# Kernel tuning notes

Hardware: AMD Instinct MI355X
Metric: run time of the kernel (lower is better)

## Reference

```python
import jax, jax.numpy as jnp
import numpy as np
from jax import lax

# ---- custom-numeric primitives matching the torch Function classes ----

def _sign1(x):
    # torch.sign with sign(0) -> 1
    return jnp.where(x >= 0, jnp.ones_like(x), -jnp.ones_like(x))

bin_act = _sign1            # BinaryActivation.forward
bin_weight = _sign1         # WeightsToBinary.forward
round_bias = jnp.round      # BiasToInt.forward

C_IN, C_OUT, K = 14, 128, 7
H_MID = 2 * K               # h = k * 2 = 14
PAD = K // 2                # 3


def _conv(x, w, b, stride, pad, groups):
    y = lax.conv_general_dilated(
        x, w,
        window_strides=(stride, stride),
        padding=((pad, pad), (pad, pad)),
        dimension_numbers=("NCHW", "OIHW", "NCHW"),
        feature_group_count=groups,
    )
    return y + b[None, :, None, None]


def setup_inputs() -> dict:
    key = jax.random.key(0)
    ks = jax.random.split(key, 7)
    B, H, W = 8, 384, 384
    x = jax.random.normal(ks[0], (B, C_IN, H, W), dtype=jnp.float32)
    # latent float weights in roughly (-1, 1) like a trained BNN
    w1 = 0.5 * jax.random.normal(ks[1], (H_MID, 1, K, K), dtype=jnp.float32)      # depthwise, groups=C_IN
    b1 = 0.5 * jax.random.normal(ks[2], (H_MID,), dtype=jnp.float32)
    w2 = 0.5 * jax.random.normal(ks[3], (C_OUT, H_MID, 1, 1), dtype=jnp.float32)
    b2 = 0.5 * jax.random.normal(ks[4], (C_OUT,), dtype=jnp.float32)
    w3 = 0.5 * jax.random.normal(ks[5], (C_OUT, C_OUT, 1, 1), dtype=jnp.float32)
    b3 = 0.5 * jax.random.normal(ks[6], (C_OUT,), dtype=jnp.float32)
    return {"x": x, "w1": w1, "b1": b1, "w2": w2, "b2": b2, "w3": w3, "b3": b3}


def reference(x, w1, b1, w2, b2, w3, b3):
    # first=True: center then binarize input
    x = bin_act(x - jnp.mean(x))
    # conv1: depthwise k x k, stride 1, padding k//2 (same spatial)
    y = bin_act(_conv(x, bin_weight(w1), round_bias(b1), 1, PAD, C_IN))
    # conv2: 1x1 conv but padding k//2 (grows spatial by 2*PAD) -- quirk of source
    y = bin_act(_conv(y, bin_weight(w2), round_bias(b2), 1, PAD, 1))
    # conv3: 1x1 conv, stride 3, padding 1
    y = bin_act(_conv(y, bin_weight(w3), round_bias(b3), 3, 1, 1))
    return y
```

## Files before the change

kernel.cpp:

```cpp
#include <hip/hip_runtime.h>
#include <hip/hip_bf16.h>

#define NB     8
#define CIN    14
#define COUT   128
#define HW     384
#define OUT_HW 131
#define P      (OUT_HW*OUT_HW)
#define ROWS   390
#define NTOT   (NB*CIN*HW*HW)
#define NROWS  (NB*CIN*ROWS)
#define NPACK  1024
#define CAND_B 0.002f
#define NSLOT  8

typedef unsigned long long u64;
typedef unsigned int u32;

struct PackedW {
    uint4 padz;
    uint4 ringz;
    u64   w1pack[CIN];
    int   b1i[CIN];
};

__global__ __launch_bounds__(256) void pass1(
    const float* __restrict__ x, u64* __restrict__ xbin,
    double* __restrict__ part, u64* __restrict__ cands, u32* __restrict__ ccnt,
    const float* __restrict__ w1, const float* __restrict__ b1,
    const float* __restrict__ w2, const float* __restrict__ b2,
    const float* __restrict__ w3, const float* __restrict__ b3,
    uint4* __restrict__ zlut, PackedW* __restrict__ pw)
{
    const int tid  = threadIdx.x;
    const int lane = tid & 63;
    const int wv   = tid >> 6;

    if (blockIdx.x < NPACK) {
        const u64 lmlt = (1ull << lane) - 1ull;
        double s0 = 0.0, s1 = 0.0;
        const int wid = blockIdx.x * 4 + wv;
        for (int row = wid; row < NROWS; row += NPACK * 4) {
            int nc = row / ROWS;
            int rr = row - nc * ROWS;
            int r  = rr - 3;
            u64 v = 0;
            u32 running = 0;
            u64* crow = cands + (size_t)row * NSLOT;
            if (r >= 0 && r < HW) {
                const float* xr = x + ((size_t)nc * HW + r) * HW;
                float f0 = __builtin_nontemporal_load(xr + lane);
                float f1 = __builtin_nontemporal_load(xr + 64 + lane);
                float f2 = __builtin_nontemporal_load(xr + 128 + lane);
                float f3 = __builtin_nontemporal_load(xr + 192 + lane);
                float f4 = __builtin_nontemporal_load(xr + 256 + lane);
                float f5 = __builtin_nontemporal_load(xr + 320 + lane);
                s0 += ((double)f0 + (double)f1) + (double)f2;
                s1 += ((double)f3 + (double)f4) + (double)f5;
                u64 b0 = __ballot(f0 >= 0.f);
                u64 b1_ = __ballot(f1 >= 0.f);
                u64 b2_ = __ballot(f2 >= 0.f);
                u64 b3_ = __ballot(f3 >= 0.f);
                u64 b4_ = __ballot(f4 >= 0.f);
                u64 b5_ = __ballot(f5 >= 0.f);
                v = lane == 0 ? b0 : lane == 1 ? b1_ : lane == 2 ? b2_ :
                    lane == 3 ? b3_ : lane == 4 ? b4_ : lane == 5 ? b5_ : 0;

                const u32 pbase = (u32)row * 512u + (u32)lane;
                float fq[6] = {f0, f1, f2, f3, f4, f5};
                #pragma unroll
                for (int q = 0; q < 6; q++) {
                    u64 cq = __ballot(__builtin_fabsf(fq[q]) < CAND_B);
                    if (cq) {
                        if (__builtin_fabsf(fq[q]) < CAND_B) {
                            u32 slot = running + (u32)__popcll(cq & lmlt);
                            if (slot < NSLOT)
                                crow[slot] = ((u64)__float_as_uint(fq[q]) << 32)
                                           | (pbase + (u32)q * 64u);
                        }
                        running += (u32)__popcll(cq);
                    }
                }
            }
            if (lane < 8) xbin[(size_t)row * 8 + lane] = (lane < 6) ? v : 0;
            if (lane == 0) ccnt[row] = (running > NSLOT) ? NSLOT : running;
        }
        double s = s0 + s1;
        for (int off = 32; off; off >>= 1) s += __shfl_down(s, off);
        __shared__ double wsum[4];
        if (lane == 0) wsum[wv] = s;
        __syncthreads();
        if (tid == 0) part[blockIdx.x] = ((wsum[0] + wsum[1]) + (wsum[2] + wsum[3]));
        return;
    }

    if (blockIdx.x < NPACK + 64) {
        __shared__ u32  sw2e[COUT];
        __shared__ uint4 sw3p[COUT];
        __shared__ int  st3[COUT];
        if (tid < COUT) {
            u32 wb = 0;
            const float* w2r = w2 + tid * CIN;
            for (int c = 0; c < CIN; c++) wb |= (u32)(w2r[c] >= 0.f) << c;
            int b2i = (int)rintf(b2[tid]);
            sw2e[tid] = wb | ((u32)((CIN + b2i) >> 1) << 16);
            st3[tid] = (COUT + (int)rintf(b3[tid])) >> 1;
        }
        {
            int co = tid >> 1, half = tid & 1;
            const float* wr = w3 + co * COUT + half * 64;
            u64 mm = 0;
            #pragma unroll 8
            for (int c = 0; c < 64; c++) mm |= (u64)(wr[c] >= 0.f) << c;
            if (half == 0) { sw3p[co].x = (u32)mm; sw3p[co].y = (u32)(mm >> 32); }
            else           { sw3p[co].z = (u32)mm; sw3p[co].w = (u32)(mm >> 32); }
        }
        __syncthreads();

        const u32 y1v = (blockIdx.x - NPACK) * 256 + tid;
        u64 y2lo = 0, y2hi = 0;
        #pragma unroll 8
        for (int co = 0; co < 64; co++) {
            u32 e = sw2e[co];
            int p = __popc((y1v ^ e) & 0x3FFFu);
            y2lo |= (u64)(p <= ((int)e >> 16)) << co;
        }
        #pragma unroll 8
        for (int co = 0; co < 64; co++) {
            u32 e = sw2e[64 + co];
            int p = __popc((y1v ^ e) & 0x3FFFu);
            y2hi |= (u64)(p <= ((int)e >> 16)) << co;
        }
        u32 z[4] = {0, 0, 0, 0};
        #pragma unroll 4
        for (int co = 0; co < COUT; co++) {
            uint4 w = sw3p[co];
            int pp = (int)(__popcll(y2lo ^ (((u64)w.y << 32) | w.x))
                         + __popcll(y2hi ^ (((u64)w.w << 32) | w.z)));
            z[co >> 5] |= (u32)(pp <= st3[co]) << (co & 31);
        }
        zlut[y1v] = make_uint4(z[0], z[1], z[2], z[3]);
        return;
    }

    {
        __shared__ u64 sBorder[2], sPad[2], sRing[2];
        __shared__ u64 sw3lo[COUT], sw3hi[COUT];
        __shared__ int sb3[COUT];
        if (tid < COUT) {
            const float* wr = w3 + tid * COUT;
            u64 lo = 0, hi = 0;
            #pragma unroll 8
            for (int c = 0; c < 64; c++) lo |= (u64)(wr[c] >= 0.f) << c;
            #pragma unroll 8
            for (int c = 0; c < 64; c++) hi |= (u64)(wr[64 + c] >= 0.f) << c;
            sw3lo[tid] = lo; sw3hi[tid] = hi;
            int b2i = (int)rintf(b2[tid]);
            int b3i = (int)rintf(b3[tid]);
            sb3[tid] = b3i;
            u64 bb2 = __ballot(b2i >= 0);
            u64 bb3 = __ballot(b3i >= 0);
            if (lane == 0) { sBorder[wv] = bb2; sPad[wv] = bb3; }
        } else {
            int q = tid - COUT;
            if (q < CIN) {
                const float* wr = w1 + q * 49;
                u64 pk = 0;
                for (int c = 0; c < 49; c++) pk |= (u64)(wr[c] >= 0.f) << c;
                pw->w1pack[q] = pk;
                pw->b1i[q] = (int)rintf(b1[q]);
            }
        }
        __syncthreads();
        if (tid < COUT) {
            int s3 = COUT + sb3[tid]
                   - 2 * (int)(__popcll(sBorder[0] ^ sw3lo[tid]) + __popcll(sBorder[1] ^ sw3hi[tid]));
            u64 rb = __ballot(s3 >= 0);
            if (lane == 0) sRing[wv] = rb;
        }
        __syncthreads();
        if (tid == 0) {
            pw->padz  = make_uint4((u32)sPad[0],  (u32)(sPad[0] >> 32),  (u32)sPad[1],  (u32)(sPad[1] >> 32));
            pw->ringz = make_uint4((u32)sRing[0], (u32)(sRing[0] >> 32), (u32)sRing[1], (u32)(sRing[1] >> 32));
        }
    }
}

__global__ __launch_bounds__(256) void bnn_row(
    const u64* __restrict__ xbin, const PackedW* __restrict__ pw,
    const uint4* __restrict__ zlut, const double* __restrict__ part,
    const u64* __restrict__ cands, const u32* __restrict__ ccnt,
    float* __restrict__ out)
{
    __shared__ u64 xrows[CIN][7][8];
    __shared__ u32 zl[4][132];
    __shared__ u64 sw1[CIN];
    __shared__ int sb1[CIN];
    __shared__ double wsum[4];

    const int tid  = threadIdx.x;
    const int lane = tid & 63;
    const int wv   = tid >> 6;
    const u32 blk  = blockIdx.x;
    const u32 n = blk / OUT_HW;
    const u32 i = blk - n * OUT_HW;
    const bool interior = (i >= 2 && i <= 129);
    const int p0 = 3 * (int)i - 4;

    if (tid < CIN) { sw1[tid] = pw->w1pack[tid]; sb1[tid] = pw->b1i[tid]; }

    if (interior) {
        double t = 0.0;
        for (int q = tid; q < NPACK; q += 256) t += part[q];
        for (int off = 32; off; off >>= 1) t += __shfl_down(t, off);
        if (lane == 0) wsum[wv] = t;

        for (int t2 = tid; t2 < CIN * 56; t2 += 256) {
            int ci  = t2 / 56;
            int rem = t2 - ci * 56;
            int dy  = rem >> 3, w = rem & 7;
            xrows[ci][dy][w] =
                xbin[(((size_t)n * CIN + ci) * ROWS + (u32)(p0 + dy)) * 8 + w];
        }
    }
    __syncthreads();

    if (interior) {
        const float m = (float)((((wsum[0] + wsum[1]) + (wsum[2] + wsum[3]))
                                 / (double)NTOT));
        if (tid < CIN * 7) {
            int ci = tid / 7, dy = tid - ci * 7;
            u32 gr = ((u32)n * CIN + (u32)ci) * ROWS + (u32)(p0 + dy);
            u32 cnt = ccnt[gr];
            for (u32 s = 0; s < cnt; s++) {
                u64 e = cands[(size_t)gr * NSLOT + s];
                float v = __uint_as_float((u32)(e >> 32));
                bool bz = (v >= 0.f), bm = (v >= m);
                if (bz != bm) {
                    u32 pos = (u32)e;
                    xrows[ci][dy][(pos >> 6) & 7] ^= 1ull << (pos & 63);
                }
            }
        }
    }
    __syncthreads();

    if (tid < OUT_HW) {
        const int j = tid;
        uint4 zz;
        if (i == 0 || j == 0) {
            zz = pw->padz;
        } else if (!interior || j == 1 || j == 130) {
            zz = pw->ringz;
        } else {
            const int c0 = 3 * j - 7;
            const int lsh = (c0 < 0) ? 1 : 0;
            const int c0c = (c0 < 0) ? 0 : c0;
            const int k   = c0c >> 6;
            const int off = c0c & 63;
            const u64 selz = off ? ~0ull : 0ull;
            const int shl1 = (64 - off) & 63;
            u32 vm = 0x7Fu;
            if (c0 < 0)    vm = 0x7Eu;
            if (c0 == 380) vm = 0x0Fu;
            u64 vmrep = (u64)vm * 0x0000040810204081ull;
            u64 rmask = (1ull << 49) - 1;
            if (p0 < 3)   rmask &= ~((1ull << (7 * (3 - p0))) - 1);
            if (p0 > 380) rmask &= (1ull << (7 * (387 - p0))) - 1;
            const u64 M = vmrep & rmask;
            const int npop = (int)__popcll(M);

            u32 y1v = 0;
            #pragma unroll
            for (int ci = 0; ci < CIN; ci++) {
                u64 bits = 0;
                #pragma unroll
                for (int dy = 0; dy < 7; dy++) {
                    u64 w0 = xrows[ci][dy][k];
                    u64 w1 = xrows[ci][dy][k + 1];
                    u64 v = (w0 >> off) | ((w1 & selz) << shl1);
                    u32 b7 = ((u32)v << lsh) & 0x7Fu;
                    bits |= (u64)b7 << (7 * dy);
                }
                int T = sb1[ci] + npop - 2 * (int)__popcll((bits ^ sw1[ci]) & M);
                y1v |= (u32)(T >= 0) << ci;
            }
            zz = zlut[y1v];
        }
        zl[0][j] = zz.x; zl[1][j] = zz.y; zl[2][j] = zz.z; zl[3][j] = zz.w;
    }
    __syncthreads();

    const size_t base = (size_t)n * COUT * P + (size_t)i * OUT_HW;
    for (int co = wv; co < COUT; co += 4) {
        const u32 b = co & 31;
        const u32* zp = zl[co >> 5];
        float* op = out + base + (size_t)co * P;
        u32 wa = zp[lane], wb = zp[64 + lane];
        op[lane]      = ((wa >> b) & 1u) ? 1.0f : -1.0f;
        op[64 + lane] = ((wb >> b) & 1u) ? 1.0f : -1.0f;
        if (lane < 3) {
            u32 wc = zp[128 + lane];
            op[128 + lane] = ((wc >> b) & 1u) ? 1.0f : -1.0f;
        }
    }
}

extern "C" void kernel_launch(void* const* d_in, const int* in_sizes, int n_in,
                              void* d_out, int out_size, void* d_ws, size_t ws_size,
                              hipStream_t stream) {
    const float* x  = (const float*)d_in[0];
    const float* w1 = (const float*)d_in[1];
    const float* b1 = (const float*)d_in[2];
    const float* w2 = (const float*)d_in[3];
    const float* b2 = (const float*)d_in[4];
    const float* w3 = (const float*)d_in[5];
    const float* b3 = (const float*)d_in[6];
    float* out = (float*)d_out;

    double*  partials = (double*)d_ws;
    PackedW* pw       = (PackedW*)((char*)d_ws + 8448);
    uint4*   zlut     = (uint4*)((char*)d_ws + 16384);
    u64*     xbin     = (u64*)((char*)d_ws + 278528);
    u64*     cands    = (u64*)((char*)d_ws + 3074048);
    u32*     ccnt     = (u32*)((char*)d_ws + 5869568);

    pass1<<<NPACK + 64 + 1, 256, 0, stream>>>(x, xbin, partials, cands, ccnt,
                                              w1, b1, w2, b2, w3, b3, zlut, pw);
    bnn_row<<<NB * OUT_HW, 256, 0, stream>>>(xbin, pw, zlut, partials,
                                             cands, ccnt, out);
}
```

Measured before the change: 51.94 us.

## Split output unpack into separate kernel with coalesced vectorized float4 stores

```diff
diff --git a/kernel.cpp b/kernel.cpp
--- a/kernel.cpp
+++ b/kernel.cpp
@@ -7,15 +7,18 @@
 #define HW     384
 #define OUT_HW 131
 #define P      (OUT_HW*OUT_HW)
+#define TOTPIX (NB*P)
 #define ROWS   390
 #define NTOT   (NB*CIN*HW*HW)
 #define NROWS  (NB*CIN*ROWS)
 #define NPACK  1024
 #define CAND_B 0.002f
 #define NSLOT  8
+#define QELT   4291
 
 typedef unsigned long long u64;
 typedef unsigned int u32;
+typedef float f4 __attribute__((ext_vector_type(4)));
 
 struct PackedW {
     uint4 padz;
@@ -186,11 +189,11 @@
     }
 }
 
-__global__ __launch_bounds__(256) void bnn_row(
+__global__ __launch_bounds__(256) void conv_zrow(
     const u64* __restrict__ xbin, const PackedW* __restrict__ pw,
     const uint4* __restrict__ zlut, const double* __restrict__ part,
     const u64* __restrict__ cands, const u32* __restrict__ ccnt,
-    float* __restrict__ out)
+    u32* __restrict__ zws)
 {
     __shared__ u64 xrows[CIN][7][8];
     __shared__ u32 zl[4][132];
@@ -291,18 +294,53 @@
     }
     __syncthreads();
 
-    const size_t base = (size_t)n * COUT * P + (size_t)i * OUT_HW;
-    for (int co = wv; co < COUT; co += 4) {
-        const u32 b = co & 31;
-        const u32* zp = zl[co >> 5];
-        float* op = out + base + (size_t)co * P;
-        u32 wa = zp[lane], wb = zp[64 + lane];
-        op[lane]      = ((wa >> b) & 1u) ? 1.0f : -1.0f;
-        op[64 + lane] = ((wb >> b) & 1u) ? 1.0f : -1.0f;
-        if (lane < 3) {
-            u32 wc = zp[128 + lane];
-            op[128 + lane] = ((wc >> b) & 1u) ? 1.0f : -1.0f;
-        }
+    const u32 rbase = n * P + i * OUT_HW;
+    for (int t = tid; t < 4 * OUT_HW; t += 256) {
+        int qq = t / OUT_HW;
+        int j  = t - qq * OUT_HW;
+        zws[(size_t)qq * TOTPIX + rbase + j] = zl[qq][j];
+    }
+}
+
+__global__ __launch_bounds__(256) void unpack4(
+    const u32* __restrict__ zws, float* __restrict__ out)
+{
+    const u32 blk = blockIdx.x;
+    const u32 q   = blk >> 2;
+    const int s   = blk & 3;
+    const int tid = threadIdx.x;
+    const u32 n  = q >> 7, co = q & 127u, b = co & 31u;
+    const u32* zp = zws + (co >> 5) * TOTPIX + n * P;
+    float* op = out + (size_t)q * P;
+
+    const int lo = s * QELT;
+    const int hi = (lo + QELT < P) ? lo + QELT : P;
+    const int mis = (int)((q * (u32)P + (u32)lo) & 3u);
+    int a0 = mis ? (4 - mis) : 0;
+    if (lo + a0 > hi) a0 = hi - lo;
+
+    if (tid < a0) {
+        u32 w = zp[lo + tid];
+        op[lo + tid] = ((w >> b) & 1u) ? 1.0f : -1.0f;
+    }
+    const int start = lo + a0;
+    const int nch = (hi - start) >> 2;
+    for (int c = tid; c < nch; c += 256) {
+        int p0 = start + 4 * c;
+        u32 w0 = zp[p0], w1 = zp[p0 + 1], w2 = zp[p0 + 2], w3 = zp[p0 + 3];
+        f4 f;
+        f.x = ((w0 >> b) & 1u) ? 1.0f : -1.0f;
+        f.y = ((w1 >> b) & 1u) ? 1.0f : -1.0f;
+        f.z = ((w2 >> b) & 1u) ? 1.0f : -1.0f;
+        f.w = ((w3 >> b) & 1u) ? 1.0f : -1.0f;
+        *(f4*)(op + p0) = f;
+    }
+    const int done = start + 4 * nch;
+    const int rem  = hi - done;
+    if (tid >= 64 && tid < 64 + rem) {
+        int pix = done + (tid - 64);
+        u32 w = zp[pix];
+        op[pix] = ((w >> b) & 1u) ? 1.0f : -1.0f;
     }
 }
 
@@ -324,9 +362,11 @@
     u64*     xbin     = (u64*)((char*)d_ws + 278528);
     u64*     cands    = (u64*)((char*)d_ws + 3074048);
     u32*     ccnt     = (u32*)((char*)d_ws + 5869568);
+    u32*     zws      = (u32*)((char*)d_ws + 6045696);
 
     pass1<<<NPACK + 64 + 1, 256, 0, stream>>>(x, xbin, partials, cands, ccnt,
                                               w1, b1, w2, b2, w3, b3, zlut, pw);
-    bnn_row<<<NB * OUT_HW, 256, 0, stream>>>(xbin, pw, zlut, partials,
-                                             cands, ccnt, out);
+    conv_zrow<<<NB * OUT_HW, 256, 0, stream>>>(xbin, pw, zlut, partials,
+                                               cands, ccnt, zws);
+    unpack4<<<NB * COUT * 4, 256, 0, stream>>>(zws, out);
 }
```

Measured after the change: 54.52 us. 5.0% more time.

## Process two output rows per block to share input row loads

Applied to the files above, without the earlier changes.

```diff
diff --git a/kernel.cpp b/kernel.cpp
--- a/kernel.cpp
+++ b/kernel.cpp
@@ -13,6 +13,7 @@
 #define NPACK  1024
 #define CAND_B 0.002f
 #define NSLOT  8
+#define NPAIR  66
 
 typedef unsigned long long u64;
 typedef unsigned int u32;
@@ -192,8 +193,8 @@
     const u64* __restrict__ cands, const u32* __restrict__ ccnt,
     float* __restrict__ out)
 {
-    __shared__ u64 xrows[CIN][7][8];
-    __shared__ u32 zl[4][132];
+    __shared__ u64 xrows[CIN][10][8];
+    __shared__ u32 zl[4][2][132];
     __shared__ u64 sw1[CIN];
     __shared__ int sb1[CIN];
     __shared__ double wsum[4];
@@ -202,35 +203,37 @@
     const int lane = tid & 63;
     const int wv   = tid >> 6;
     const u32 blk  = blockIdx.x;
-    const u32 n = blk / OUT_HW;
-    const u32 i = blk - n * OUT_HW;
-    const bool interior = (i >= 2 && i <= 129);
-    const int p0 = 3 * (int)i - 4;
+    const u32 n  = blk / NPAIR;
+    const u32 ig = blk - n * NPAIR;
+    const int i0 = 2 * (int)ig;
+    const int nv = (i0 + 1 <= 130) ? 2 : 1;
+    const bool anyInt = (ig >= 1 && ig <= 64);
+    const int ps = 3 * i0 - 4;
 
     if (tid < CIN) { sw1[tid] = pw->w1pack[tid]; sb1[tid] = pw->b1i[tid]; }
 
-    if (interior) {
+    if (anyInt) {
         double t = 0.0;
         for (int q = tid; q < NPACK; q += 256) t += part[q];
         for (int off = 32; off; off >>= 1) t += __shfl_down(t, off);
         if (lane == 0) wsum[wv] = t;
 
-        for (int t2 = tid; t2 < CIN * 56; t2 += 256) {
-            int ci  = t2 / 56;
-            int rem = t2 - ci * 56;
+        for (int t2 = tid; t2 < CIN * 80; t2 += 256) {
+            int ci  = t2 / 80;
+            int rem = t2 - ci * 80;
             int dy  = rem >> 3, w = rem & 7;
             xrows[ci][dy][w] =
-                xbin[(((size_t)n * CIN + ci) * ROWS + (u32)(p0 + dy)) * 8 + w];
+                xbin[(((size_t)n * CIN + ci) * ROWS + (u32)(ps + dy)) * 8 + w];
         }
     }
     __syncthreads();
 
-    if (interior) {
+    if (anyInt) {
         const float m = (float)((((wsum[0] + wsum[1]) + (wsum[2] + wsum[3]))
                                  / (double)NTOT));
-        if (tid < CIN * 7) {
-            int ci = tid / 7, dy = tid - ci * 7;
-            u32 gr = ((u32)n * CIN + (u32)ci) * ROWS + (u32)(p0 + dy);
+        if (tid < CIN * 10) {
+            int ci = tid / 10, dy = tid - ci * 10;
+            u32 gr = ((u32)n * CIN + (u32)ci) * ROWS + (u32)(ps + dy);
             u32 cnt = ccnt[gr];
             for (u32 s = 0; s < cnt; s++) {
                 u64 e = cands[(size_t)gr * NSLOT + s];
@@ -245,14 +248,18 @@
     }
     __syncthreads();
 
-    if (tid < OUT_HW) {
-        const int j = tid;
+    for (int t = tid; t < nv * OUT_HW; t += 256) {
+        const int di = (t >= OUT_HW) ? 1 : 0;
+        const int j  = t - di * OUT_HW;
+        const int i  = i0 + di;
+        const bool interiorI = (i >= 2 && i <= 129);
         uint4 zz;
         if (i == 0 || j == 0) {
             zz = pw->padz;
-        } else if (!interior || j == 1 || j == 130) {
+        } else if (!interiorI || j == 1 || j == 130) {
             zz = pw->ringz;
         } else {
+            const int p0 = 3 * i - 4;
             const int c0 = 3 * j - 7;
             const int lsh = (c0 < 0) ? 1 : 0;
             const int c0c = (c0 < 0) ? 0 : c0;
@@ -269,6 +276,7 @@
             if (p0 > 380) rmask &= (1ull << (7 * (387 - p0))) - 1;
             const u64 M = vmrep & rmask;
             const int npop = (int)__popcll(M);
+            const int dyb = 3 * di;
 
             u32 y1v = 0;
             #pragma unroll
@@ -276,8 +284,8 @@
                 u64 bits = 0;
                 #pragma unroll
                 for (int dy = 0; dy < 7; dy++) {
-                    u64 w0 = xrows[ci][dy][k];
-                    u64 w1 = xrows[ci][dy][k + 1];
+                    u64 w0 = xrows[ci][dyb + dy][k];
+                    u64 w1 = xrows[ci][dyb + dy][k + 1];
                     u64 v = (w0 >> off) | ((w1 & selz) << shl1);
                     u32 b7 = ((u32)v << lsh) & 0x7Fu;
                     bits |= (u64)b7 << (7 * dy);
@@ -287,21 +295,22 @@
             }
             zz = zlut[y1v];
         }
-        zl[0][j] = zz.x; zl[1][j] = zz.y; zl[2][j] = zz.z; zl[3][j] = zz.w;
+        zl[0][di][j] = zz.x; zl[1][di][j] = zz.y;
+        zl[2][di][j] = zz.z; zl[3][di][j] = zz.w;
     }
     __syncthreads();
 
-    const size_t base = (size_t)n * COUT * P + (size_t)i * OUT_HW;
+    const size_t base = (size_t)n * COUT * P + (size_t)i0 * OUT_HW;
+    const int tot = nv * OUT_HW;
     for (int co = wv; co < COUT; co += 4) {
         const u32 b = co & 31;
-        const u32* zp = zl[co >> 5];
+        const u32* zp = &zl[co >> 5][0][0];
         float* op = out + base + (size_t)co * P;
-        u32 wa = zp[lane], wb = zp[64 + lane];
-        op[lane]      = ((wa >> b) & 1u) ? 1.0f : -1.0f;
-        op[64 + lane] = ((wb >> b) & 1u) ? 1.0f : -1.0f;
-        if (lane < 3) {
-            u32 wc = zp[128 + lane];
-            op[128 + lane] = ((wc >> b) & 1u) ? 1.0f : -1.0f;
+        for (int t = lane; t < tot; t += 64) {
+            const int di = (t >= OUT_HW) ? 1 : 0;
+            const int j  = t - di * OUT_HW;
+            u32 w = zp[di * 132 + j];
+            op[t] = ((w >> b) & 1u) ? 1.0f : -1.0f;
         }
     }
 }
@@ -327,6 +336,6 @@
 
     pass1<<<NPACK + 64 + 1, 256, 0, stream>>>(x, xbin, partials, cands, ccnt,
                                               w1, b1, w2, b2, w3, b3, zlut, pw);
-    bnn_row<<<NB * OUT_HW, 256, 0, stream>>>(xbin, pw, zlut, partials,
-                                             cands, ccnt, out);
+    bnn_row<<<NB * NPAIR, 256, 0, stream>>>(xbin, pw, zlut, partials,
+                                            cands, ccnt, out);
 }
```

After: 58.26 us. +12.2%, slower.
